# Performance work log

Measured on AMD Instinct MI355X. Metric: run time of the kernel, lower is better.

The kernel has to match this reference:

```python
import jax, jax.numpy as jnp
import numpy as np

B, N1, N2, D, O = 4, 256, 256, 64, 64
TEMP = 1.0
BN_EPS = 1e-5


def setup_inputs() -> dict:
    key = jax.random.key(0)
    ks = jax.random.split(key, 24)
    s = lambda n: 1.0 / np.sqrt(n)
    inp = {
        'x1': jax.random.normal(ks[0], (B, N1, D), jnp.float32),
        'x2': jax.random.normal(ks[1], (B, N2, D), jnp.float32),
        'W_t1': jax.random.normal(ks[2], (D, D), jnp.float32) * s(D),
        'b_t1': jnp.zeros((D,), jnp.float32),
        'W_t2': jax.random.normal(ks[3], (D, D), jnp.float32) * s(D),
        'b_t2': jnp.zeros((D,), jnp.float32),
        'W_att': jax.random.normal(ks[4], (D, O), jnp.float32) * s(D),
        'b_att': jnp.zeros((O,), jnp.float32),
        'W_attM': jax.random.normal(ks[5], (D, O), jnp.float32) * s(D),
        'b_attM': jnp.zeros((O,), jnp.float32),
        'w11': jax.random.normal(ks[6], (O, 1), jnp.float32) * s(O),
        'w22': jax.random.normal(ks[7], (O, 1), jnp.float32) * s(O),
        'w12': jax.random.normal(ks[8], (O, 1), jnp.float32) * s(O),
        'wM': jax.random.normal(ks[9], (O, 1), jnp.float32) * s(O),
        'W_pa': jax.random.normal(ks[10], (D, O), jnp.float32) * s(D),
        'b_pa': jnp.zeros((O,), jnp.float32),
        'W_po': jax.random.normal(ks[11], (D, O), jnp.float32) * s(D),
        'b_po': jnp.zeros((O,), jnp.float32),
        'W_paM': jax.random.normal(ks[12], (D, O), jnp.float32) * s(D),
        'b_paM': jnp.zeros((O,), jnp.float32),
        'W_poM': jax.random.normal(ks[13], (D, O), jnp.float32) * s(D),
        'b_poM': jnp.zeros((O,), jnp.float32),
        'gamma': jnp.ones((O,), jnp.float32),
        'beta': jnp.zeros((O,), jnp.float32),
    }
    return inp


def _forward(x1, x2, W_t1, b_t1, W_t2, b_t2, W_att, b_att, W_attM, b_attM,
             w11, w22, w12, wM, W_pa, b_pa, W_po, b_po, W_paM, b_paM,
             W_poM, b_poM, gamma, beta):
    n1 = x1.shape[1]
    h1 = x1 @ W_t1 + b_t1                      # (B,n1,D)
    h2 = x2 @ W_t2 + b_t2                      # (B,n2,D)
    x = jnp.concatenate([h1, h2], axis=1)      # (B,N,D)
    master = jnp.mean(x, axis=1, keepdims=True)  # (B,1,D)

    # --- type-blocked attention map ---
    pair = x[:, :, None, :] * x[:, None, :, :]          # (B,N,N,D)
    e = jnp.tanh(pair @ W_att + b_att)                   # (B,N,N,O)
    s11 = jnp.einsum('bijd,d->bij', e[:, :n1, :n1], w11[:, 0])
    s12 = jnp.einsum('bijd,d->bij', e[:, :n1, n1:], w12[:, 0])
    s21 = jnp.einsum('bijd,d->bij', e[:, n1:, :n1], w12[:, 0])
    s22 = jnp.einsum('bijd,d->bij', e[:, n1:, n1:], w22[:, 0])
    top = jnp.concatenate([s11, s12], axis=2)
    bot = jnp.concatenate([s21, s22], axis=2)
    scores = jnp.concatenate([top, bot], axis=1)         # (B,N,N)
    att = jax.nn.softmax(scores / TEMP, axis=2)          # softmax over source nodes (torch dim=-2 of (B,N,N,1))

    # --- master update ---
    m = jnp.tanh((x * master) @ W_attM + b_attM)         # (B,N,O)
    aM = jax.nn.softmax((m @ wM) / TEMP, axis=1)         # (B,N,1)
    agg_m = jnp.einsum('bn,bnd->bd', aM[:, :, 0], x)[:, None, :]  # (B,1,D)
    master_new = (agg_m @ W_paM + b_paM) + (master @ W_poM + b_poM)

    # --- node projection + BN(eval) + SELU ---
    agg = jnp.einsum('bij,bjd->bid', att, x)             # (B,N,D)
    y = (agg @ W_pa + b_pa) + (x @ W_po + b_po)          # (B,N,O)
    y = y / jnp.sqrt(1.0 + BN_EPS) * gamma + beta        # BN eval: mean=0, var=1
    y = jax.nn.selu(y)
    return y[:, :n1], y[:, n1:], master_new


def reference(x1, x2, W_t1, b_t1, W_t2, b_t2, W_att, b_att, W_attM, b_attM,
              w11, w22, w12, wM, W_pa, b_pa, W_po, b_po, W_paM, b_paM,
              W_poM, b_poM, gamma, beta):
    return _forward(x1, x2, W_t1, b_t1, W_t2, b_t2, W_att, b_att, W_attM,
                    b_attM, w11, w22, w12, wM, W_pa, b_pa, W_po, b_po,
                    W_paM, b_paM, W_poM, b_poM, gamma, beta)
```

## Files before the change

### kernel.cpp

```cpp
#include <hip/hip_runtime.h>

#define BB 4
#define NN 512
#define NH 256
#define DD 64

typedef __attribute__((ext_vector_type(8))) short bf16x8;
typedef __attribute__((ext_vector_type(16))) float f32x16;
union BF8 { bf16x8 v; unsigned int u[4]; };

__device__ __forceinline__ float wred_sum(float v) {
  v += __shfl_xor(v, 32);
  v += __shfl_xor(v, 16);
  v += __shfl_xor(v, 8);
  v += __shfl_xor(v, 4);
  v += __shfl_xor(v, 2);
  v += __shfl_xor(v, 1);
  return v;
}

__device__ __forceinline__ float wred_max(float v) {
  v = fmaxf(v, __shfl_xor(v, 32));
  v = fmaxf(v, __shfl_xor(v, 16));
  v = fmaxf(v, __shfl_xor(v, 8));
  v = fmaxf(v, __shfl_xor(v, 4));
  v = fmaxf(v, __shfl_xor(v, 2));
  v = fmaxf(v, __shfl_xor(v, 1));
  return v;
}

__device__ __forceinline__ unsigned int cvtpk_bf16(float lo, float hi) {
  unsigned int r;
  asm("v_cvt_pk_bf16_f32 %0, %1, %2" : "=v"(r) : "v"(lo), "v"(hi));
  return r;
}

__device__ __forceinline__ float fast_exp2(float x) {
  float r;
  asm("v_exp_f32 %0, %1" : "=v"(r) : "v"(x));
  return r;
}

__device__ __forceinline__ float fast_tanh(float t) {
  t = fminf(15.f, fmaxf(-15.f, t));
  float z = __expf(2.f * t);
  return 1.f - 2.f * __builtin_amdgcn_rcpf(z + 1.f);
}

__global__ __launch_bounds__(256)
void k1_build_x(const float* __restrict__ x1, const float* __restrict__ x2,
                const float* __restrict__ W_t1, const float* __restrict__ b_t1,
                const float* __restrict__ W_t2, const float* __restrict__ b_t2,
                float* __restrict__ X) {
  const int tid = threadIdx.x;
  const int lane = tid & 63;
  const int rq = tid >> 6;
  const int r = blockIdx.x * 4 + rq;
  const int b = r >> 9;
  const int n = r & 511;
  const float* src; const float* W; const float* bias;
  if (n < NH) { src = x1 + (b * NH + n) * DD;        W = W_t1; bias = b_t1; }
  else        { src = x2 + (b * NH + (n - NH)) * DD; W = W_t2; bias = b_t2; }
  const float4* s4 = reinterpret_cast<const float4*>(src);
  float t0 = 0.f, t1 = 0.f, t2 = 0.f, t3 = 0.f;
#pragma unroll
  for (int c = 0; c < 16; ++c) {
    const float4 v = s4[c];
    t0 = fmaf(v.x, W[(4 * c + 0) * DD + lane], t0);
    t1 = fmaf(v.y, W[(4 * c + 1) * DD + lane], t1);
    t2 = fmaf(v.z, W[(4 * c + 2) * DD + lane], t2);
    t3 = fmaf(v.w, W[(4 * c + 3) * DD + lane], t3);
  }
  X[r * DD + lane] = ((t0 + t1) + (t2 + t3)) + bias[lane];
}

__global__ __launch_bounds__(1024, 4)
void k3_fused(const float* __restrict__ X,
              const float* __restrict__ W_att, const float* __restrict__ b_att,
              const float* __restrict__ w11, const float* __restrict__ w22,
              const float* __restrict__ w12,
              const float* __restrict__ W_attM, const float* __restrict__ b_attM,
              const float* __restrict__ wM,
              const float* __restrict__ W_pa, const float* __restrict__ b_pa,
              const float* __restrict__ W_po, const float* __restrict__ b_po,
              const float* __restrict__ gamma, const float* __restrict__ beta,
              float* __restrict__ master, float* __restrict__ logits,
              float* __restrict__ out) {
  const int b = blockIdx.y;
  const int i0 = blockIdx.x * 8;
  const int tid = threadIdx.x;
  const int lane = tid & 63;
  const int w = tid >> 6;
  const int l31 = lane & 31;
  const int half = lane >> 5;
  const int j0 = w << 5;

  __shared__ __align__(16) float Xlds[NN * DD];
  __shared__ __align__(16) float sc[8 * NN];
  __shared__ __align__(16) float red2[16][DD];
  __shared__ __align__(16) float aggL[8][DD];
  __shared__ __align__(16) float tblB[64];
  __shared__ __align__(16) float tblW[2][64];
  __shared__ __align__(16) float mastL[64];

  const float* __restrict__ Xb = X + b * NN * DD;
  const float K2E = 2.8853900817779268f;
  const int itype = (i0 >= NH);
  const int jtype = (w >= 8);

  {
    const int c4 = (tid & 15) * 4;
    const int rh = tid >> 4;
#pragma unroll
    for (int it = 0; it < 8; ++it) {
      const int r = it * 64 + rh;
      *reinterpret_cast<float4*>(&Xlds[r * DD + c4]) =
          *reinterpret_cast<const float4*>(&Xb[r * DD + c4]);
    }
  }
  if (tid < 64) {
    const int ot = tid >> 5, hf = (tid >> 4) & 1, r = tid & 15;
    const int o = ot * 32 + (r & 3) + 8 * (r >> 2) + 4 * hf;
    tblB[tid] = K2E * b_att[o];
  } else if (tid >= 128 && tid < 256) {
    const int t = tid - 128;
    const int jt = t >> 6;
    const int idx = t & 63;
    const int ot = idx >> 5, hf = (idx >> 4) & 1, r = idx & 15;
    const int o = ot * 32 + (r & 3) + 8 * (r >> 2) + 4 * hf;
    const float* wsl = itype ? (jt ? w22 : w12) : (jt ? w12 : w11);
    tblW[jt][idx] = -2.f * wsl[o];
  }

  BF8 Wp[2][4];
#pragma unroll
  for (int ot = 0; ot < 2; ++ot)
#pragma unroll
    for (int kt = 0; kt < 4; ++kt) {
      const int o = ot * 32 + l31;
#pragma unroll
      for (int p = 0; p < 4; ++p) {
        const int d0 = kt * 16 + half * 8 + 2 * p;
        Wp[ot][kt].u[p] = cvtpk_bf16(W_att[d0 * DD + o], W_att[(d0 + 1) * DD + o]);
      }
    }

  BF8 Xf[4];
#pragma unroll
  for (int kt = 0; kt < 4; ++kt) {
    const float* base = Xb + (j0 + l31) * DD + kt * 16 + half * 8;
    const float4 a = *reinterpret_cast<const float4*>(base);
    const float4 c = *reinterpret_cast<const float4*>(base + 4);
    Xf[kt].u[0] = cvtpk_bf16(a.x, a.y);
    Xf[kt].u[1] = cvtpk_bf16(a.z, a.w);
    Xf[kt].u[2] = cvtpk_bf16(c.x, c.y);
    Xf[kt].u[3] = cvtpk_bf16(c.z, c.w);
  }

  const float* wsel = itype ? (jtype ? w22 : w12) : (jtype ? w12 : w11);
  const float swv = wred_sum(wsel[lane]);

  __syncthreads();

  {
    float s = 0.f;
    for (int r = w * 32; r < w * 32 + 32; ++r) s += Xlds[r * DD + lane];
    red2[w][lane] = s;
  }
  __syncthreads();
  if (w == 0) {
    float s = 0.f;
#pragma unroll
    for (int k = 0; k < 16; ++k) s += red2[k][lane];
    s *= (1.f / 512.f);
    mastL[lane] = s;
    if (blockIdx.x == 0) master[b * DD + lane] = s;
  }

#pragma unroll 1
  for (int ii = 0; ii < 8; ++ii) {
    BF8 Bi[4];
#pragma unroll
    for (int kt = 0; kt < 4; ++kt) {
      const float4 xa = *reinterpret_cast<const float4*>(&Xlds[(i0 + ii) * DD + kt * 16 + half * 8]);
      const float4 xc = *reinterpret_cast<const float4*>(&Xlds[(i0 + ii) * DD + kt * 16 + half * 8 + 4]);
      unsigned int u;
      u = Xf[kt].u[0];
      Bi[kt].u[0] = cvtpk_bf16(xa.x * __uint_as_float(u << 16),
                               xa.y * __uint_as_float(u & 0xffff0000u));
      u = Xf[kt].u[1];
      Bi[kt].u[1] = cvtpk_bf16(xa.z * __uint_as_float(u << 16),
                               xa.w * __uint_as_float(u & 0xffff0000u));
      u = Xf[kt].u[2];
      Bi[kt].u[2] = cvtpk_bf16(xc.x * __uint_as_float(u << 16),
                               xc.y * __uint_as_float(u & 0xffff0000u));
      u = Xf[kt].u[3];
      Bi[kt].u[3] = cvtpk_bf16(xc.z * __uint_as_float(u << 16),
                               xc.w * __uint_as_float(u & 0xffff0000u));
    }
    float ptot = 0.f;
#pragma unroll
    for (int ot = 0; ot < 2; ++ot) {
      f32x16 C = {};
#pragma unroll
      for (int kt = 0; kt < 4; ++kt)
        C = __builtin_amdgcn_mfma_f32_32x32x16_bf16(Wp[ot][kt].v, Bi[kt].v, C, 0, 0, 0);
      const int base = ot * 32 + half * 16;
      float p = 0.f;
#pragma unroll
      for (int r = 0; r < 16; ++r) {
        const float arg = fmaf(C[r], K2E, tblB[base + r]);
        const float e = fast_exp2(arg);
        p = fmaf(tblW[jtype][base + r], __builtin_amdgcn_rcpf(e + 1.f), p);
      }
      ptot += p;
    }
    ptot += __shfl_xor(ptot, 32);
    if (lane < 32) sc[ii * NN + j0 + l31] = swv + ptot;
  }
  __syncthreads();

  const int row = w & 7, part = w >> 3;
  const int irow = i0 + row;
  float v[8];
#pragma unroll
  for (int k = 0; k < 8; ++k) v[k] = sc[row * NN + lane + 64 * k];
  __syncthreads();
  float mx = fmaxf(fmaxf(fmaxf(v[0], v[1]), fmaxf(v[2], v[3])),
                   fmaxf(fmaxf(v[4], v[5]), fmaxf(v[6], v[7])));
  mx = wred_max(mx);
  float ssum = 0.f;
#pragma unroll
  for (int k = 0; k < 8; ++k) { v[k] = __expf(v[k] - mx); ssum += v[k]; }
  ssum = wred_sum(ssum);
  const float inv = __builtin_amdgcn_rcpf(ssum);
#pragma unroll
  for (int k = 0; k < 4; ++k) {
    const int kk = part * 4 + k;
    sc[row * NN + lane + 64 * kk] = v[kk] * inv;
  }

  float a0 = 0.f, a1 = 0.f, a2 = 0.f, a3 = 0.f;
  const float* scr = &sc[row * NN + part * 256];
  const int xof = part * 256 * DD;
  for (int jj = 0; jj < 64; ++jj) {
    const float4 at = *reinterpret_cast<const float4*>(&scr[jj * 4]);
    a0 = fmaf(at.x, Xlds[xof + (jj * 4 + 0) * DD + lane], a0);
    a1 = fmaf(at.y, Xlds[xof + (jj * 4 + 1) * DD + lane], a1);
    a2 = fmaf(at.z, Xlds[xof + (jj * 4 + 2) * DD + lane], a2);
    a3 = fmaf(at.w, Xlds[xof + (jj * 4 + 3) * DD + lane], a3);
  }
  red2[w][lane] = (a0 + a1) + (a2 + a3);
  __syncthreads();

  if (part == 0) {
    const float aggv = red2[w][lane] + red2[w + 8][lane];
    aggL[row][lane] = aggv;
    float y = b_pa[lane] + b_po[lane];
#pragma unroll 8
    for (int d = 0; d < DD; ++d) {
      y = fmaf(aggL[row][d], W_pa[d * DD + lane], y);
      y = fmaf(Xlds[irow * DD + d], W_po[d * DD + lane], y);
    }
    const float RSQ = 0.9999950000374997f;
    y = y * RSQ * gamma[lane] + beta[lane];
    const float SC_ = 1.0507009873554805f;
    const float AL = 1.6732632423543772f;
    y = (y > 0.f) ? (SC_ * y) : (SC_ * AL * (__expf(y) - 1.f));
    const int off = (irow < NH) ? ((b * NH + irow) * DD + lane)
                                : (BB * NH * DD + (b * NH + (irow - NH)) * DD + lane);
    out[off] = y;
  } else {
    float lg = b_attM[lane];
#pragma unroll 8
    for (int d = 0; d < DD; ++d)
      lg = fmaf(Xlds[irow * DD + d] * mastL[d], W_attM[d * DD + lane], lg);
    const float th = fast_tanh(lg);
    const float s = wred_sum(th * wM[lane]);
    if (lane == 0) logits[b * NN + irow] = s;
  }
}

__global__ __launch_bounds__(256)
void k4_master_new(const float* __restrict__ X, const float* __restrict__ master,
                   const float* __restrict__ logits,
                   const float* __restrict__ W_paM, const float* __restrict__ b_paM,
                   const float* __restrict__ W_poM, const float* __restrict__ b_poM,
                   float* __restrict__ out) {
  const int b = blockIdx.x;
  const int tid = threadIdx.x;
  const int lane = tid & 63;
  const int q = tid >> 6;
  __shared__ float red[4][DD];
  __shared__ float r4[4];
  __shared__ float aggm_s[DD];
  __shared__ float mrow_s[DD];
  const float* lg = logits + b * NN;
  const float v0 = lg[tid];
  const float v1 = lg[tid + 256];
  float mx = wred_max(fmaxf(v0, v1));
  if (lane == 0) r4[q] = mx;
  __syncthreads();
  mx = fmaxf(fmaxf(r4[0], r4[1]), fmaxf(r4[2], r4[3]));
  float es = __expf(v0 - mx) + __expf(v1 - mx);
  es = wred_sum(es);
  __syncthreads();
  if (lane == 0) r4[q] = es;
  __syncthreads();
  const float S = r4[0] + r4[1] + r4[2] + r4[3];
  const float invS = 1.f / S;

  float acc = 0.f;
  for (int nn = q * 128; nn < q * 128 + 128; ++nn) {
    const float a = __expf(lg[nn] - mx);
    acc = fmaf(a, X[(b * NN + nn) * DD + lane], acc);
  }
  red[q][lane] = acc;
  __syncthreads();
  if (q == 0) {
    aggm_s[lane] =
        (red[0][lane] + red[1][lane] + red[2][lane] + red[3][lane]) * invS;
    mrow_s[lane] = master[b * DD + lane];
  }
  __syncthreads();
  float p = 0.f;
  for (int d = q * 16; d < q * 16 + 16; ++d) {
    p = fmaf(aggm_s[d], W_paM[d * DD + lane], p);
    p = fmaf(mrow_s[d], W_poM[d * DD + lane], p);
  }
  __syncthreads();
  red[q][lane] = p;
  __syncthreads();
  if (q == 0) {
    out[2 * BB * NH * DD + b * DD + lane] =
        red[0][lane] + red[1][lane] + red[2][lane] + red[3][lane] +
        b_paM[lane] + b_poM[lane];
  }
}

extern "C" void kernel_launch(void* const* d_in, const int* in_sizes, int n_in,
                              void* d_out, int out_size, void* d_ws, size_t ws_size,
                              hipStream_t stream) {
  const float* x1    = (const float*)d_in[0];
  const float* x2    = (const float*)d_in[1];
  const float* W_t1  = (const float*)d_in[2];
  const float* b_t1  = (const float*)d_in[3];
  const float* W_t2  = (const float*)d_in[4];
  const float* b_t2  = (const float*)d_in[5];
  const float* W_att = (const float*)d_in[6];
  const float* b_att = (const float*)d_in[7];
  const float* W_attM = (const float*)d_in[8];
  const float* b_attM = (const float*)d_in[9];
  const float* w11   = (const float*)d_in[10];
  const float* w22   = (const float*)d_in[11];
  const float* w12   = (const float*)d_in[12];
  const float* wM    = (const float*)d_in[13];
  const float* W_pa  = (const float*)d_in[14];
  const float* b_pa  = (const float*)d_in[15];
  const float* W_po  = (const float*)d_in[16];
  const float* b_po  = (const float*)d_in[17];
  const float* W_paM = (const float*)d_in[18];
  const float* b_paM = (const float*)d_in[19];
  const float* W_poM = (const float*)d_in[20];
  const float* b_poM = (const float*)d_in[21];
  const float* gamma = (const float*)d_in[22];
  const float* beta  = (const float*)d_in[23];

  float* ws     = (float*)d_ws;
  float* X      = ws;
  float* master = ws + 131072;
  float* logits = ws + 131328;
  float* out    = (float*)d_out;

  k1_build_x<<<512, 256, 0, stream>>>(x1, x2, W_t1, b_t1, W_t2, b_t2, X);
  k3_fused<<<dim3(64, 4), 1024, 0, stream>>>(X, W_att, b_att, w11, w22, w12,
                                             W_attM, b_attM, wM, W_pa, b_pa,
                                             W_po, b_po, gamma, beta,
                                             master, logits, out);
  k4_master_new<<<4, 256, 0, stream>>>(X, master, logits, W_paM, b_paM, W_poM, b_poM, out);
}
```

Before: 52.11 us.

## Split fused attention kernel into score kernel and aggregation kernel

Moves pairwise score computation into a separate kernel with 512 blocks of 4 query rows each, keeping bf16 X and W_att in swizzled LDS instead of registers. Scores go through a global scratch buffer, and a second kernel does the softmax, aggregation and projection. The aim is more parallelism and lower register and LDS pressure in the MFMA-heavy phase. The cost is an extra launch plus a global round trip for the 4x512x512 score matrix.

Result: slower. 63.52 us (+21.9%).

```diff
diff --git a/kernel.cpp b/kernel.cpp
--- a/kernel.cpp
+++ b/kernel.cpp
@@ -8,6 +8,7 @@
 typedef __attribute__((ext_vector_type(8))) short bf16x8;
 typedef __attribute__((ext_vector_type(16))) float f32x16;
 union BF8 { bf16x8 v; unsigned int u[4]; };
+union BF8Q { bf16x8 v; uint4 q; };
 
 __device__ __forceinline__ float wred_sum(float v) {
   v += __shfl_xor(v, 32);
@@ -46,6 +47,9 @@
   float z = __expf(2.f * t);
   return 1.f - 2.f * __builtin_amdgcn_rcpf(z + 1.f);
 }
+
+__device__ __forceinline__ float bflo(unsigned int u) { return __uint_as_float(u << 16); }
+__device__ __forceinline__ float bfhi(unsigned int u) { return __uint_as_float(u & 0xffff0000u); }
 
 __global__ __launch_bounds__(256)
 void k1_build_x(const float* __restrict__ x1, const float* __restrict__ x2,
@@ -74,11 +78,128 @@
   X[r * DD + lane] = ((t0 + t1) + (t2 + t3)) + bias[lane];
 }
 
+__global__ __launch_bounds__(1024, 8)
+void k3a_scores(const float* __restrict__ X,
+                const float* __restrict__ W_att, const float* __restrict__ b_att,
+                const float* __restrict__ w11, const float* __restrict__ w22,
+                const float* __restrict__ w12,
+                float* __restrict__ scG) {
+  const int b = blockIdx.y;
+  const int i0 = blockIdx.x * 4;
+  const int tid = threadIdx.x;
+  const int lane = tid & 63;
+  const int w = tid >> 6;
+  const int l31 = lane & 31;
+  const int half = lane >> 5;
+  const int j0 = w << 5;
+
+  __shared__ __align__(16) unsigned int XtU[NN * 32];
+  __shared__ __align__(16) unsigned int WpL[8 * 64 * 4];
+  __shared__ __align__(16) float tblB[64];
+  __shared__ __align__(16) float tblW[2][64];
+
+  const float* __restrict__ Xb = X + b * NN * DD;
+  const float K2E = 2.8853900817779268f;
+  const int itype = (i0 >= NH);
+  const int jtype = (w >= 8);
+
+  {
+    const int j = tid >> 1;
+    const int dh = (tid & 1) * 32;
+    const float4* src = reinterpret_cast<const float4*>(&Xb[j * DD + dh]);
+#pragma unroll
+    for (int s4 = 0; s4 < 4; ++s4) {
+      const float4 a = src[s4 * 2];
+      const float4 c = src[s4 * 2 + 1];
+      uint4 v;
+      v.x = cvtpk_bf16(a.x, a.y);
+      v.y = cvtpk_bf16(a.z, a.w);
+      v.z = cvtpk_bf16(c.x, c.y);
+      v.w = cvtpk_bf16(c.z, c.w);
+      const int slot = (dh >> 3) + s4;
+      const unsigned int ba = (unsigned int)((j * 128 + slot * 16) ^ ((j & 7) << 4));
+      *reinterpret_cast<uint4*>(reinterpret_cast<char*>(XtU) + ba) = v;
+    }
+  }
+  if (w < 8) {
+    const int ot = w >> 2, kt = w & 3;
+    const int o = ot * 32 + l31;
+    uint4 v;
+#pragma unroll
+    for (int p = 0; p < 4; ++p) {
+      const int d0 = kt * 16 + half * 8 + 2 * p;
+      const unsigned int pk = cvtpk_bf16(W_att[d0 * DD + o], W_att[(d0 + 1) * DD + o]);
+      if (p == 0) v.x = pk; else if (p == 1) v.y = pk; else if (p == 2) v.z = pk; else v.w = pk;
+    }
+    *reinterpret_cast<uint4*>(&WpL[(w * 64 + lane) * 4]) = v;
+  }
+  if (tid < 64) {
+    const int ot = tid >> 5, hf = (tid >> 4) & 1, r = tid & 15;
+    const int o = ot * 32 + (r & 3) + 8 * (r >> 2) + 4 * hf;
+    tblB[tid] = K2E * b_att[o];
+  } else if (tid >= 128 && tid < 256) {
+    const int t = tid - 128;
+    const int jt = t >> 6;
+    const int idx = t & 63;
+    const int ot = idx >> 5, hf = (idx >> 4) & 1, r = idx & 15;
+    const int o = ot * 32 + (r & 3) + 8 * (r >> 2) + 4 * hf;
+    const float* wsl = itype ? (jt ? w22 : w12) : (jt ? w12 : w11);
+    tblW[jt][idx] = -2.f * wsl[o];
+  }
+
+  const float* wsel = itype ? (jtype ? w22 : w12) : (jtype ? w12 : w11);
+  const float swv = wred_sum(wsel[lane]);
+
+  const int jrow = j0 + l31;
+  unsigned int addrXt[4];
+#pragma unroll
+  for (int kt = 0; kt < 4; ++kt)
+    addrXt[kt] = (unsigned int)((jrow * 128 + kt * 32 + half * 16) ^ ((jrow & 7) << 4));
+
+  __syncthreads();
+
+#pragma unroll 1
+  for (int ii = 0; ii < 4; ++ii) {
+    f32x16 C0 = {}, C1 = {};
+#pragma unroll
+    for (int kt = 0; kt < 4; ++kt) {
+      const uint4 xj = *reinterpret_cast<const uint4*>(
+          reinterpret_cast<const char*>(XtU) + addrXt[kt]);
+      const float4 xa = *reinterpret_cast<const float4*>(&Xb[(i0 + ii) * DD + kt * 16 + half * 8]);
+      const float4 xc = *reinterpret_cast<const float4*>(&Xb[(i0 + ii) * DD + kt * 16 + half * 8 + 4]);
+      BF8 Bi;
+      Bi.u[0] = cvtpk_bf16(xa.x * bflo(xj.x), xa.y * bfhi(xj.x));
+      Bi.u[1] = cvtpk_bf16(xa.z * bflo(xj.y), xa.w * bfhi(xj.y));
+      Bi.u[2] = cvtpk_bf16(xc.x * bflo(xj.z), xc.y * bfhi(xj.z));
+      Bi.u[3] = cvtpk_bf16(xc.z * bflo(xj.w), xc.w * bfhi(xj.w));
+      BF8Q wf0, wf1;
+      wf0.q = *reinterpret_cast<const uint4*>(&WpL[((0 * 4 + kt) * 64 + lane) * 4]);
+      wf1.q = *reinterpret_cast<const uint4*>(&WpL[((1 * 4 + kt) * 64 + lane) * 4]);
+      C0 = __builtin_amdgcn_mfma_f32_32x32x16_bf16(wf0.v, Bi.v, C0, 0, 0, 0);
+      C1 = __builtin_amdgcn_mfma_f32_32x32x16_bf16(wf1.v, Bi.v, C1, 0, 0, 0);
+    }
+    float p0a = 0.f, p0b = 0.f, p1a = 0.f, p1b = 0.f;
+    const int base = half * 16;
+#pragma unroll
+    for (int r = 0; r < 16; ++r) {
+      const float arg0 = fmaf(C0[r], K2E, tblB[base + r]);
+      const float e0 = fast_exp2(arg0);
+      if (r & 1) p0a = fmaf(tblW[jtype][base + r], __builtin_amdgcn_rcpf(e0 + 1.f), p0a);
+      else       p0b = fmaf(tblW[jtype][base + r], __builtin_amdgcn_rcpf(e0 + 1.f), p0b);
+      const float arg1 = fmaf(C1[r], K2E, tblB[32 + base + r]);
+      const float e1 = fast_exp2(arg1);
+      if (r & 1) p1a = fmaf(tblW[jtype][32 + base + r], __builtin_amdgcn_rcpf(e1 + 1.f), p1a);
+      else       p1b = fmaf(tblW[jtype][32 + base + r], __builtin_amdgcn_rcpf(e1 + 1.f), p1b);
+    }
+    float ptot = (p0a + p0b) + (p1a + p1b);
+    ptot += __shfl_xor(ptot, 32);
+    if (lane < 32)
+      scG[(b * NN + i0 + ii) * NN + j0 + l31] = swv + ptot;
+  }
+}
+
 __global__ __launch_bounds__(1024, 4)
-void k3_fused(const float* __restrict__ X,
-              const float* __restrict__ W_att, const float* __restrict__ b_att,
-              const float* __restrict__ w11, const float* __restrict__ w22,
-              const float* __restrict__ w12,
+void k3b_rest(const float* __restrict__ X, const float* __restrict__ scG,
               const float* __restrict__ W_attM, const float* __restrict__ b_attM,
               const float* __restrict__ wM,
               const float* __restrict__ W_pa, const float* __restrict__ b_pa,
@@ -91,22 +212,14 @@
   const int tid = threadIdx.x;
   const int lane = tid & 63;
   const int w = tid >> 6;
-  const int l31 = lane & 31;
-  const int half = lane >> 5;
-  const int j0 = w << 5;
 
   __shared__ __align__(16) float Xlds[NN * DD];
-  __shared__ __align__(16) float sc[8 * NN];
+  __shared__ __align__(16) float scL[8 * NN];
   __shared__ __align__(16) float red2[16][DD];
   __shared__ __align__(16) float aggL[8][DD];
-  __shared__ __align__(16) float tblB[64];
-  __shared__ __align__(16) float tblW[2][64];
   __shared__ __align__(16) float mastL[64];
 
   const float* __restrict__ Xb = X + b * NN * DD;
-  const float K2E = 2.8853900817779268f;
-  const int itype = (i0 >= NH);
-  const int jtype = (w >= 8);
 
   {
     const int c4 = (tid & 15) * 4;
@@ -118,48 +231,12 @@
           *reinterpret_cast<const float4*>(&Xb[r * DD + c4]);
     }
   }
-  if (tid < 64) {
-    const int ot = tid >> 5, hf = (tid >> 4) & 1, r = tid & 15;
-    const int o = ot * 32 + (r & 3) + 8 * (r >> 2) + 4 * hf;
-    tblB[tid] = K2E * b_att[o];
-  } else if (tid >= 128 && tid < 256) {
-    const int t = tid - 128;
-    const int jt = t >> 6;
-    const int idx = t & 63;
-    const int ot = idx >> 5, hf = (idx >> 4) & 1, r = idx & 15;
-    const int o = ot * 32 + (r & 3) + 8 * (r >> 2) + 4 * hf;
-    const float* wsl = itype ? (jt ? w22 : w12) : (jt ? w12 : w11);
-    tblW[jt][idx] = -2.f * wsl[o];
-  }
-
-  BF8 Wp[2][4];
-#pragma unroll
-  for (int ot = 0; ot < 2; ++ot)
-#pragma unroll
-    for (int kt = 0; kt < 4; ++kt) {
-      const int o = ot * 32 + l31;
-#pragma unroll
-      for (int p = 0; p < 4; ++p) {
-        const int d0 = kt * 16 + half * 8 + 2 * p;
-        Wp[ot][kt].u[p] = cvtpk_bf16(W_att[d0 * DD + o], W_att[(d0 + 1) * DD + o]);
-      }
-    }
-
-  BF8 Xf[4];
-#pragma unroll
-  for (int kt = 0; kt < 4; ++kt) {
-    const float* base = Xb + (j0 + l31) * DD + kt * 16 + half * 8;
-    const float4 a = *reinterpret_cast<const float4*>(base);
-    const float4 c = *reinterpret_cast<const float4*>(base + 4);
-    Xf[kt].u[0] = cvtpk_bf16(a.x, a.y);
-    Xf[kt].u[1] = cvtpk_bf16(a.z, a.w);
-    Xf[kt].u[2] = cvtpk_bf16(c.x, c.y);
-    Xf[kt].u[3] = cvtpk_bf16(c.z, c.w);
-  }
-
-  const float* wsel = itype ? (jtype ? w22 : w12) : (jtype ? w12 : w11);
-  const float swv = wred_sum(wsel[lane]);
-
+  {
+    const int r8 = tid >> 7;
+    const int c = (tid & 127) * 4;
+    *reinterpret_cast<float4*>(&scL[r8 * NN + c]) =
+        *reinterpret_cast<const float4*>(&scG[(b * NN + i0 + r8) * NN + c]);
+  }
   __syncthreads();
 
   {
@@ -177,54 +254,11 @@
     if (blockIdx.x == 0) master[b * DD + lane] = s;
   }
 
-#pragma unroll 1
-  for (int ii = 0; ii < 8; ++ii) {
-    BF8 Bi[4];
-#pragma unroll
-    for (int kt = 0; kt < 4; ++kt) {
-      const float4 xa = *reinterpret_cast<const float4*>(&Xlds[(i0 + ii) * DD + kt * 16 + half * 8]);
-      const float4 xc = *reinterpret_cast<const float4*>(&Xlds[(i0 + ii) * DD + kt * 16 + half * 8 + 4]);
-      unsigned int u;
-      u = Xf[kt].u[0];
-      Bi[kt].u[0] = cvtpk_bf16(xa.x * __uint_as_float(u << 16),
-                               xa.y * __uint_as_float(u & 0xffff0000u));
-      u = Xf[kt].u[1];
-      Bi[kt].u[1] = cvtpk_bf16(xa.z * __uint_as_float(u << 16),
-                               xa.w * __uint_as_float(u & 0xffff0000u));
-      u = Xf[kt].u[2];
-      Bi[kt].u[2] = cvtpk_bf16(xc.x * __uint_as_float(u << 16),
-                               xc.y * __uint_as_float(u & 0xffff0000u));
-      u = Xf[kt].u[3];
-      Bi[kt].u[3] = cvtpk_bf16(xc.z * __uint_as_float(u << 16),
-                               xc.w * __uint_as_float(u & 0xffff0000u));
-    }
-    float ptot = 0.f;
-#pragma unroll
-    for (int ot = 0; ot < 2; ++ot) {
-      f32x16 C = {};
-#pragma unroll
-      for (int kt = 0; kt < 4; ++kt)
-        C = __builtin_amdgcn_mfma_f32_32x32x16_bf16(Wp[ot][kt].v, Bi[kt].v, C, 0, 0, 0);
-      const int base = ot * 32 + half * 16;
-      float p = 0.f;
-#pragma unroll
-      for (int r = 0; r < 16; ++r) {
-        const float arg = fmaf(C[r], K2E, tblB[base + r]);
-        const float e = fast_exp2(arg);
-        p = fmaf(tblW[jtype][base + r], __builtin_amdgcn_rcpf(e + 1.f), p);
-      }
-      ptot += p;
-    }
-    ptot += __shfl_xor(ptot, 32);
-    if (lane < 32) sc[ii * NN + j0 + l31] = swv + ptot;
-  }
-  __syncthreads();
-
   const int row = w & 7, part = w >> 3;
   const int irow = i0 + row;
   float v[8];
 #pragma unroll
-  for (int k = 0; k < 8; ++k) v[k] = sc[row * NN + lane + 64 * k];
+  for (int k = 0; k < 8; ++k) v[k] = scL[row * NN + lane + 64 * k];
   __syncthreads();
   float mx = fmaxf(fmaxf(fmaxf(v[0], v[1]), fmaxf(v[2], v[3])),
                    fmaxf(fmaxf(v[4], v[5]), fmaxf(v[6], v[7])));
@@ -237,11 +271,11 @@
 #pragma unroll
   for (int k = 0; k < 4; ++k) {
     const int kk = part * 4 + k;
-    sc[row * NN + lane + 64 * kk] = v[kk] * inv;
+    scL[row * NN + lane + 64 * kk] = v[kk] * inv;
   }
 
   float a0 = 0.f, a1 = 0.f, a2 = 0.f, a3 = 0.f;
-  const float* scr = &sc[row * NN + part * 256];
+  const float* scr = &scL[row * NN + part * 256];
   const int xof = part * 256 * DD;
   for (int jj = 0; jj < 64; ++jj) {
     const float4 at = *reinterpret_cast<const float4*>(&scr[jj * 4]);
@@ -370,12 +404,13 @@
   float* X      = ws;
   float* master = ws + 131072;
   float* logits = ws + 131328;
+  float* scG    = ws + 133376;
   float* out    = (float*)d_out;
 
   k1_build_x<<<512, 256, 0, stream>>>(x1, x2, W_t1, b_t1, W_t2, b_t2, X);
-  k3_fused<<<dim3(64, 4), 1024, 0, stream>>>(X, W_att, b_att, w11, w22, w12,
-                                             W_attM, b_attM, wM, W_pa, b_pa,
-                                             W_po, b_po, gamma, beta,
+  k3a_scores<<<dim3(128, 4), 1024, 0, stream>>>(X, W_att, b_att, w11, w22, w12, scG);
+  k3b_rest<<<dim3(64, 4), 1024, 0, stream>>>(X, scG, W_attM, b_attM, wM,
+                                             W_pa, b_pa, W_po, b_po, gamma, beta,
                                              master, logits, out);
   k4_master_new<<<4, 256, 0, stream>>>(X, master, logits, W_paM, b_paM, W_poM, b_poM, out);
 }
```

## Store X as swizzled bf16 in LDS and split fused kernel into 512-thread blocks

Applied to the files above, without the earlier changes.

Stages X in shared memory as bf16 with an XOR swizzle instead of fp32, halving LDS footprint. Blocks drop from 1024 to 512 threads and handle 4 rows each, so the grid doubles to 128x4. The pair operand is now built from LDS reads for both i and j rather than register-cached j rows, and the softmax is split across two waves through small shared reductions. The smaller LDS use and blocks aim to raise occupancy and parallelism, at the cost of extra LDS traffic, an extra barrier, and bf16 rounding of X in the aggregation and projections.

Measured after the change: 64.79 us. 1.24x slower.

```diff
diff --git a/kernel.cpp b/kernel.cpp
--- a/kernel.cpp
+++ b/kernel.cpp
@@ -8,6 +8,7 @@
 typedef __attribute__((ext_vector_type(8))) short bf16x8;
 typedef __attribute__((ext_vector_type(16))) float f32x16;
 union BF8 { bf16x8 v; unsigned int u[4]; };
+union BF8Q { bf16x8 v; uint4 q; };
 
 __device__ __forceinline__ float wred_sum(float v) {
   v += __shfl_xor(v, 32);
@@ -45,6 +46,13 @@
   t = fminf(15.f, fmaxf(-15.f, t));
   float z = __expf(2.f * t);
   return 1.f - 2.f * __builtin_amdgcn_rcpf(z + 1.f);
+}
+
+__device__ __forceinline__ float bflo(unsigned int u) { return __uint_as_float(u << 16); }
+__device__ __forceinline__ float bfhi(unsigned int u) { return __uint_as_float(u & 0xffff0000u); }
+
+__device__ __forceinline__ unsigned int xswz(int row, int byte_in_row) {
+  return (unsigned int)((row * 128 + byte_in_row) ^ ((row & 7) << 4));
 }
 
 __global__ __launch_bounds__(256)
@@ -74,7 +82,7 @@
   X[r * DD + lane] = ((t0 + t1) + (t2 + t3)) + bias[lane];
 }
 
-__global__ __launch_bounds__(1024, 4)
+__global__ __launch_bounds__(512, 1)
 void k3_fused(const float* __restrict__ X,
               const float* __restrict__ W_att, const float* __restrict__ b_att,
               const float* __restrict__ w11, const float* __restrict__ w22,
@@ -87,35 +95,42 @@
               float* __restrict__ master, float* __restrict__ logits,
               float* __restrict__ out) {
   const int b = blockIdx.y;
-  const int i0 = blockIdx.x * 8;
+  const int i0 = blockIdx.x * 4;
   const int tid = threadIdx.x;
   const int lane = tid & 63;
   const int w = tid >> 6;
   const int l31 = lane & 31;
   const int half = lane >> 5;
-  const int j0 = w << 5;
-
-  __shared__ __align__(16) float Xlds[NN * DD];
-  __shared__ __align__(16) float sc[8 * NN];
+  const int j0 = w << 6;
+
+  __shared__ __align__(16) unsigned int Xbf[NN * 32];
+  __shared__ __align__(16) float sc[4 * NN];
   __shared__ __align__(16) float red2[16][DD];
-  __shared__ __align__(16) float aggL[8][DD];
+  __shared__ __align__(16) float aggL[4][DD];
   __shared__ __align__(16) float tblB[64];
   __shared__ __align__(16) float tblW[2][64];
   __shared__ __align__(16) float mastL[64];
+  __shared__ __align__(16) float smax[8];
+  __shared__ __align__(16) float ssum8[8];
 
   const float* __restrict__ Xb = X + b * NN * DD;
   const float K2E = 2.8853900817779268f;
   const int itype = (i0 >= NH);
-  const int jtype = (w >= 8);
+  const int jtype = (w >= 4);
 
   {
-    const int c4 = (tid & 15) * 4;
-    const int rh = tid >> 4;
-#pragma unroll
-    for (int it = 0; it < 8; ++it) {
-      const int r = it * 64 + rh;
-      *reinterpret_cast<float4*>(&Xlds[r * DD + c4]) =
-          *reinterpret_cast<const float4*>(&Xb[r * DD + c4]);
+    const int r = tid;
+    const float4* src = reinterpret_cast<const float4*>(&Xb[r * DD]);
+#pragma unroll
+    for (int s = 0; s < 8; ++s) {
+      const float4 a = src[s * 2];
+      const float4 c = src[s * 2 + 1];
+      uint4 v;
+      v.x = cvtpk_bf16(a.x, a.y);
+      v.y = cvtpk_bf16(a.z, a.w);
+      v.z = cvtpk_bf16(c.x, c.y);
+      v.w = cvtpk_bf16(c.z, c.w);
+      *reinterpret_cast<uint4*>(reinterpret_cast<char*>(Xbf) + xswz(r, s * 16)) = v;
     }
   }
   if (tid < 64) {
@@ -145,27 +160,21 @@
       }
     }
 
-  BF8 Xf[4];
-#pragma unroll
-  for (int kt = 0; kt < 4; ++kt) {
-    const float* base = Xb + (j0 + l31) * DD + kt * 16 + half * 8;
-    const float4 a = *reinterpret_cast<const float4*>(base);
-    const float4 c = *reinterpret_cast<const float4*>(base + 4);
-    Xf[kt].u[0] = cvtpk_bf16(a.x, a.y);
-    Xf[kt].u[1] = cvtpk_bf16(a.z, a.w);
-    Xf[kt].u[2] = cvtpk_bf16(c.x, c.y);
-    Xf[kt].u[3] = cvtpk_bf16(c.z, c.w);
-  }
-
   const float* wsel = itype ? (jtype ? w22 : w12) : (jtype ? w12 : w11);
   const float swv = wred_sum(wsel[lane]);
 
   __syncthreads();
 
   {
-    float s = 0.f;
-    for (int r = w * 32; r < w * 32 + 32; ++r) s += Xlds[r * DD + lane];
-    red2[w][lane] = s;
+    float se = 0.f, so = 0.f;
+    const int r0 = w * 32 + half * 256;
+    for (int r = r0; r < r0 + 32; ++r) {
+      const unsigned int u = *reinterpret_cast<const unsigned int*>(
+          reinterpret_cast<const char*>(Xbf) + xswz(r, l31 * 4));
+      se += bflo(u); so += bfhi(u);
+    }
+    float2 pr; pr.x = se; pr.y = so;
+    *reinterpret_cast<float2*>(&red2[w * 2 + half][l31 * 2]) = pr;
   }
   __syncthreads();
   if (w == 0) {
@@ -178,89 +187,100 @@
   }
 
 #pragma unroll 1
-  for (int ii = 0; ii < 8; ++ii) {
-    BF8 Bi[4];
-#pragma unroll
-    for (int kt = 0; kt < 4; ++kt) {
-      const float4 xa = *reinterpret_cast<const float4*>(&Xlds[(i0 + ii) * DD + kt * 16 + half * 8]);
-      const float4 xc = *reinterpret_cast<const float4*>(&Xlds[(i0 + ii) * DD + kt * 16 + half * 8 + 4]);
-      unsigned int u;
-      u = Xf[kt].u[0];
-      Bi[kt].u[0] = cvtpk_bf16(xa.x * __uint_as_float(u << 16),
-                               xa.y * __uint_as_float(u & 0xffff0000u));
-      u = Xf[kt].u[1];
-      Bi[kt].u[1] = cvtpk_bf16(xa.z * __uint_as_float(u << 16),
-                               xa.w * __uint_as_float(u & 0xffff0000u));
-      u = Xf[kt].u[2];
-      Bi[kt].u[2] = cvtpk_bf16(xc.x * __uint_as_float(u << 16),
-                               xc.y * __uint_as_float(u & 0xffff0000u));
-      u = Xf[kt].u[3];
-      Bi[kt].u[3] = cvtpk_bf16(xc.z * __uint_as_float(u << 16),
-                               xc.w * __uint_as_float(u & 0xffff0000u));
-    }
-    float ptot = 0.f;
-#pragma unroll
-    for (int ot = 0; ot < 2; ++ot) {
-      f32x16 C = {};
-#pragma unroll
-      for (int kt = 0; kt < 4; ++kt)
-        C = __builtin_amdgcn_mfma_f32_32x32x16_bf16(Wp[ot][kt].v, Bi[kt].v, C, 0, 0, 0);
-      const int base = ot * 32 + half * 16;
+  for (int ii = 0; ii < 4; ++ii) {
+    const int irow = i0 + ii;
+#pragma unroll
+    for (int jt = 0; jt < 2; ++jt) {
+      f32x16 C0 = {}, C1 = {};
+#pragma unroll
+      for (int kt = 0; kt < 4; ++kt) {
+        const uint4 xiu = *reinterpret_cast<const uint4*>(
+            reinterpret_cast<const char*>(Xbf) + xswz(irow, (2 * kt + half) * 16));
+        const int jrow = j0 + jt * 32 + l31;
+        const uint4 xju = *reinterpret_cast<const uint4*>(
+            reinterpret_cast<const char*>(Xbf) + xswz(jrow, (2 * kt + half) * 16));
+        BF8 Bi;
+        Bi.u[0] = cvtpk_bf16(bflo(xiu.x) * bflo(xju.x), bfhi(xiu.x) * bfhi(xju.x));
+        Bi.u[1] = cvtpk_bf16(bflo(xiu.y) * bflo(xju.y), bfhi(xiu.y) * bfhi(xju.y));
+        Bi.u[2] = cvtpk_bf16(bflo(xiu.z) * bflo(xju.z), bfhi(xiu.z) * bfhi(xju.z));
+        Bi.u[3] = cvtpk_bf16(bflo(xiu.w) * bflo(xju.w), bfhi(xiu.w) * bfhi(xju.w));
+        C0 = __builtin_amdgcn_mfma_f32_32x32x16_bf16(Wp[0][kt].v, Bi.v, C0, 0, 0, 0);
+        C1 = __builtin_amdgcn_mfma_f32_32x32x16_bf16(Wp[1][kt].v, Bi.v, C1, 0, 0, 0);
+      }
       float p = 0.f;
+      const int base = half * 16;
 #pragma unroll
       for (int r = 0; r < 16; ++r) {
-        const float arg = fmaf(C[r], K2E, tblB[base + r]);
-        const float e = fast_exp2(arg);
-        p = fmaf(tblW[jtype][base + r], __builtin_amdgcn_rcpf(e + 1.f), p);
+        const float a0 = fmaf(C0[r], K2E, tblB[base + r]);
+        const float e0 = fast_exp2(a0);
+        p = fmaf(tblW[jtype][base + r], __builtin_amdgcn_rcpf(e0 + 1.f), p);
+        const float a1 = fmaf(C1[r], K2E, tblB[32 + base + r]);
+        const float e1 = fast_exp2(a1);
+        p = fmaf(tblW[jtype][32 + base + r], __builtin_amdgcn_rcpf(e1 + 1.f), p);
       }
-      ptot += p;
-    }
-    ptot += __shfl_xor(ptot, 32);
-    if (lane < 32) sc[ii * NN + j0 + l31] = swv + ptot;
-  }
-  __syncthreads();
-
-  const int row = w & 7, part = w >> 3;
+      p += __shfl_xor(p, 32);
+      if (lane < 32) sc[ii * NN + j0 + jt * 32 + l31] = swv + p;
+    }
+  }
+  __syncthreads();
+
+  const int row = w & 3, part = w >> 2;
   const int irow = i0 + row;
-  float v[8];
-#pragma unroll
-  for (int k = 0; k < 8; ++k) v[k] = sc[row * NN + lane + 64 * k];
-  __syncthreads();
-  float mx = fmaxf(fmaxf(fmaxf(v[0], v[1]), fmaxf(v[2], v[3])),
-                   fmaxf(fmaxf(v[4], v[5]), fmaxf(v[6], v[7])));
+  float v[4];
+#pragma unroll
+  for (int k = 0; k < 4; ++k) v[k] = sc[row * NN + part * 256 + 64 * k + lane];
+  float mx = fmaxf(fmaxf(v[0], v[1]), fmaxf(v[2], v[3]));
   mx = wred_max(mx);
-  float ssum = 0.f;
-#pragma unroll
-  for (int k = 0; k < 8; ++k) { v[k] = __expf(v[k] - mx); ssum += v[k]; }
-  ssum = wred_sum(ssum);
-  const float inv = __builtin_amdgcn_rcpf(ssum);
-#pragma unroll
-  for (int k = 0; k < 4; ++k) {
-    const int kk = part * 4 + k;
-    sc[row * NN + lane + 64 * kk] = v[kk] * inv;
-  }
-
-  float a0 = 0.f, a1 = 0.f, a2 = 0.f, a3 = 0.f;
-  const float* scr = &sc[row * NN + part * 256];
-  const int xof = part * 256 * DD;
-  for (int jj = 0; jj < 64; ++jj) {
-    const float4 at = *reinterpret_cast<const float4*>(&scr[jj * 4]);
-    a0 = fmaf(at.x, Xlds[xof + (jj * 4 + 0) * DD + lane], a0);
-    a1 = fmaf(at.y, Xlds[xof + (jj * 4 + 1) * DD + lane], a1);
-    a2 = fmaf(at.z, Xlds[xof + (jj * 4 + 2) * DD + lane], a2);
-    a3 = fmaf(at.w, Xlds[xof + (jj * 4 + 3) * DD + lane], a3);
-  }
-  red2[w][lane] = (a0 + a1) + (a2 + a3);
-  __syncthreads();
+  if (lane == 0) smax[w] = mx;
+  __syncthreads();
+  mx = fmaxf(smax[w], smax[w ^ 4]);
+  float es = 0.f;
+#pragma unroll
+  for (int k = 0; k < 4; ++k) { v[k] = __expf(v[k] - mx); es += v[k]; }
+  es = wred_sum(es);
+  if (lane == 0) ssum8[w] = es;
+  __syncthreads();
+  const float inv = __builtin_amdgcn_rcpf(ssum8[w] + ssum8[w ^ 4]);
+#pragma unroll
+  for (int k = 0; k < 4; ++k) sc[row * NN + part * 256 + 64 * k + lane] = v[k] * inv;
+
+  {
+    float ae = 0.f, ao = 0.f;
+    const int jb = part * 256 + half * 128;
+    for (int jj = 0; jj < 128; ++jj) {
+      const int j = jb + jj;
+      const float at = sc[row * NN + j];
+      const unsigned int u = *reinterpret_cast<const unsigned int*>(
+          reinterpret_cast<const char*>(Xbf) + xswz(j, l31 * 4));
+      ae = fmaf(at, bflo(u), ae);
+      ao = fmaf(at, bfhi(u), ao);
+    }
+    float2 pr; pr.x = ae; pr.y = ao;
+    *reinterpret_cast<float2*>(&red2[8 * part + 2 * row + half][l31 * 2]) = pr;
+  }
+  __syncthreads();
+
+  uint4 xr[8];
+#pragma unroll
+  for (int s = 0; s < 8; ++s)
+    xr[s] = *reinterpret_cast<const uint4*>(
+        reinterpret_cast<const char*>(Xbf) + xswz(irow, s * 16));
 
   if (part == 0) {
-    const float aggv = red2[w][lane] + red2[w + 8][lane];
+    const float aggv = red2[2 * row][lane] + red2[2 * row + 1][lane] +
+                       red2[8 + 2 * row][lane] + red2[8 + 2 * row + 1][lane];
     aggL[row][lane] = aggv;
     float y = b_pa[lane] + b_po[lane];
-#pragma unroll 8
-    for (int d = 0; d < DD; ++d) {
-      y = fmaf(aggL[row][d], W_pa[d * DD + lane], y);
-      y = fmaf(Xlds[irow * DD + d], W_po[d * DD + lane], y);
+#pragma unroll
+    for (int s = 0; s < 8; ++s) {
+      const float xd[8] = {bflo(xr[s].x), bfhi(xr[s].x), bflo(xr[s].y), bfhi(xr[s].y),
+                           bflo(xr[s].z), bfhi(xr[s].z), bflo(xr[s].w), bfhi(xr[s].w)};
+#pragma unroll
+      for (int q = 0; q < 8; ++q) {
+        const int d = s * 8 + q;
+        y = fmaf(aggL[row][d], W_pa[d * DD + lane], y);
+        y = fmaf(xd[q], W_po[d * DD + lane], y);
+      }
     }
     const float RSQ = 0.9999950000374997f;
     y = y * RSQ * gamma[lane] + beta[lane];
@@ -272,9 +292,16 @@
     out[off] = y;
   } else {
     float lg = b_attM[lane];
-#pragma unroll 8
-    for (int d = 0; d < DD; ++d)
-      lg = fmaf(Xlds[irow * DD + d] * mastL[d], W_attM[d * DD + lane], lg);
+#pragma unroll
+    for (int s = 0; s < 8; ++s) {
+      const float xd[8] = {bflo(xr[s].x), bfhi(xr[s].x), bflo(xr[s].y), bfhi(xr[s].y),
+                           bflo(xr[s].z), bfhi(xr[s].z), bflo(xr[s].w), bfhi(xr[s].w)};
+#pragma unroll
+      for (int q = 0; q < 8; ++q) {
+        const int d = s * 8 + q;
+        lg = fmaf(xd[q] * mastL[d], W_attM[d * DD + lane], lg);
+      }
+    }
     const float th = fast_tanh(lg);
     const float s = wred_sum(th * wM[lane]);
     if (lane == 0) logits[b * NN + irow] = s;
@@ -373,7 +400,7 @@
   float* out    = (float*)d_out;
 
   k1_build_x<<<512, 256, 0, stream>>>(x1, x2, W_t1, b_t1, W_t2, b_t2, X);
-  k3_fused<<<dim3(64, 4), 1024, 0, stream>>>(X, W_att, b_att, w11, w22, w12,
+  k3_fused<<<dim3(128, 4), 512, 0, stream>>>(X, W_att, b_att, w11, w22, w12,
                                              W_attM, b_attM, wM, W_pa, b_pa,
                                              W_po, b_po, gamma, beta,
                                              master, logits, out);
```
